# Kernel optimization log

Hardware: AMD Instinct MI355X
Metric: run time of the kernel (lower is better)

The kernel has to match this reference:

```python
import jax, jax.numpy as jnp
import numpy as np

B, T, D_IN, D_OUT, H = 4, 2048, 768, 768, 12
HD = D_OUT // H  # 64


def setup_inputs() -> dict:
    key = jax.random.key(0)
    ks = jax.random.split(key, 6)
    s_in = 1.0 / np.sqrt(D_IN)
    s_out = 1.0 / np.sqrt(D_OUT)
    return {
        "x": jax.random.normal(ks[0], (B, T, D_IN), dtype=jnp.float32),
        "Wq": jax.random.uniform(ks[1], (D_IN, D_OUT), jnp.float32, -s_in, s_in),
        "Wk": jax.random.uniform(ks[2], (D_IN, D_OUT), jnp.float32, -s_in, s_in),
        "Wv": jax.random.uniform(ks[3], (D_IN, D_OUT), jnp.float32, -s_in, s_in),
        "Wo": jax.random.uniform(ks[4], (D_OUT, D_OUT), jnp.float32, -s_out, s_out),
        "bo": jax.random.uniform(ks[5], (D_OUT,), jnp.float32, -s_out, s_out),
    }


def reference(x, Wq, Wk, Wv, Wo, bo):
    b, t, _ = x.shape
    # QKV projections (no bias, per qkv_bias=False), split into heads: [b,h,t,hd]
    q = (x @ Wq).reshape(b, t, H, HD).transpose(0, 2, 1, 3)
    k = (x @ Wk).reshape(b, t, H, HD).transpose(0, 2, 1, 3)
    v = (x @ Wv).reshape(b, t, H, HD).transpose(0, 2, 1, 3)
    # NOTE: original calls masked_fill (non-in-place) and discards the result,
    # so NO causal mask is actually applied. Faithfully reproduce that.
    scores = jnp.einsum("bhqd,bhkd->bhqk", q, k)  # [b,h,t,t]
    attn = jax.nn.softmax(scores / jnp.sqrt(jnp.float32(HD)), axis=-1)
    # dropout p=0.0 (eval) -> identity
    ctx = jnp.einsum("bhqk,bhkd->bhqd", attn, v)  # [b,h,t,hd]
    ctx = ctx.transpose(0, 2, 1, 3).reshape(b, t, D_OUT)
    return ctx @ Wo + bo
```

## Files before the change

### kernel.cpp

```cpp
#include <hip/hip_runtime.h>
#include <hip/hip_bf16.h>
#include <stdint.h>


#define HH   12
#define TT   2048
#define DIN  768
#define DOUT 768
#define HD   64
#define BB   4
#define MTOT (BB*TT)
#define NQKV (3*DOUT)
#define QSCALE 0.1803368801111832f

typedef float  float4v  __attribute__((ext_vector_type(4)));
typedef float  float16v __attribute__((ext_vector_type(16)));
typedef __bf16 bf16x8   __attribute__((ext_vector_type(8)));
typedef short  short8v  __attribute__((ext_vector_type(8)));

#define AS1 __attribute__((address_space(1)))
#define AS3 __attribute__((address_space(3)))

static __device__ __forceinline__ void gload_lds16(const void* g, void* l) {
    __builtin_amdgcn_global_load_lds((AS1 void*)g, (AS3 void*)l, 16, 0, 0);
}

static __device__ __forceinline__ short f2bf(float f) {
    __bf16 h = (__bf16)f;
    return __builtin_bit_cast(short, h);
}

__global__ __launch_bounds__(256) void prep_kernel(const float* __restrict__ x,
                                                   const float* __restrict__ Wq,
                                                   const float* __restrict__ Wk,
                                                   const float* __restrict__ Wv,
                                                   const float* __restrict__ Wo,
                                                   short* __restrict__ Xb,
                                                   short* __restrict__ Wqkvt,
                                                   short* __restrict__ Wot) {
    __shared__ short tile[32 * 33];
    const int bx = blockIdx.x, by = blockIdx.y, bz = blockIdx.z;
    if (bz == 4) {
        const int n4 = MTOT * DIN / 4;
        const int base = (by * 24 + bx) * 256 + threadIdx.x;
        for (int i = base; i < n4; i += 24 * 24 * 256) {
            float4 v = ((const float4*)x)[i];
            short4 o;
            o.x = f2bf(v.x); o.y = f2bf(v.y); o.z = f2bf(v.z); o.w = f2bf(v.w);
            ((short4*)Xb)[i] = o;
        }
        return;
    }
    const float* W = (bz == 0) ? Wq : (bz == 1) ? Wk : (bz == 2) ? Wv : Wo;
    const int tx = threadIdx.x & 31, ty = threadIdx.x >> 5;
    for (int i = 0; i < 4; i++) {
        int k = by * 32 + ty + i * 8;
        tile[(ty + i * 8) * 33 + tx] = f2bf(W[(size_t)k * DOUT + bx * 32 + tx]);
    }
    __syncthreads();
    for (int i = 0; i < 4; i++) {
        int n = bx * 32 + ty + i * 8;
        int k = by * 32 + tx;
        short v = tile[tx * 33 + ty + i * 8];
        if (bz < 3) Wqkvt[(size_t)(bz * DOUT + n) * DIN + k] = v;
        else        Wot[(size_t)n * DOUT + k] = v;
    }
}

__global__ __launch_bounds__(256) void qkv_gemm_kernel(const short* __restrict__ Xb,
                                                       const short* __restrict__ Wt,
                                                       short* __restrict__ Qb,
                                                       short* __restrict__ Kb,
                                                       short* __restrict__ Vt) {
    __shared__ __align__(16) short lds[16384];
    short* ldsA = lds;
    short* ldsB = lds + 8192;
    const int t = threadIdx.x;
    const int w = t >> 6, lane = t & 63;
    const int quad = lane >> 4, l15 = lane & 15;
    const int m0 = blockIdx.x * 128, n0 = blockIdx.y * 128;
    const int wm = (w >> 1) * 64, wn = (w & 1) * 64;

    float4v acc[4][4];
    for (int i = 0; i < 4; i++)
        for (int j = 0; j < 4; j++)
            acc[i][j] = (float4v)0.0f;

    int sOff[4];
    int sRow[4];
#pragma unroll
    for (int g = 0; g < 4; g++) {
        int slot = g * 256 + t;
        int row = slot >> 3, ch = slot & 7;
        sRow[g] = row;
        sOff[g] = ((ch ^ (row & 7)) * 8);
    }
    const int pos_r = 0;

    for (int k0 = 0; k0 < DIN; k0 += 64) {
#pragma unroll
        for (int g = 0; g < 4; g++)
            gload_lds16(Xb + (size_t)(m0 + sRow[g]) * DIN + k0 + sOff[g], &ldsA[(g * 256 + t) * 8]);
#pragma unroll
        for (int g = 0; g < 4; g++)
            gload_lds16(Wt + (size_t)(n0 + sRow[g]) * DIN + k0 + sOff[g], &ldsB[(g * 256 + t) * 8]);
        __syncthreads();
#pragma unroll
        for (int f = 0; f < 2; f++) {
            bf16x8 af[4], bfr[4];
            for (int i = 0; i < 4; i++) {
                int row = wm + i * 16 + l15;
                af[i] = *(const bf16x8*)&ldsA[row * 64 + (((f * 4 + quad) ^ (row & 7)) * 8)];
            }
            for (int j = 0; j < 4; j++) {
                int row = wn + j * 16 + l15;
                bfr[j] = *(const bf16x8*)&ldsB[row * 64 + (((f * 4 + quad) ^ (row & 7)) * 8)];
            }
            for (int i = 0; i < 4; i++)
                for (int j = 0; j < 4; j++)
                    acc[i][j] = __builtin_amdgcn_mfma_f32_16x16x32_bf16(af[i], bfr[j], acc[i][j], 0, 0, 0);
        }
        __syncthreads();
    }
    (void)pos_r;

    const int which = n0 / DOUT;
    if (which < 2) {
        short* ldsT = lds;
        const float sc = (which == 0) ? QSCALE : 1.0f;
        short* dst = (which == 0) ? Qb : Kb;
        const int n0sec = n0 - which * DOUT;
        for (int i = 0; i < 4; i++)
            for (int j = 0; j < 4; j++) {
                int col = wn + j * 16 + l15;
                int cx = col >> 3, co = col & 7;
                for (int r = 0; r < 4; r++) {
                    int row = wm + i * 16 + quad * 4 + r;
                    ldsT[row * 128 + ((cx ^ (row & 7)) * 8 + co)] = f2bf(acc[i][j][r] * sc);
                }
            }
        __syncthreads();
        for (int p = 0; p < 8; p++) {
            int row = p * 16 + (t >> 4);
            int cL = t & 15;
            short8v v = *(const short8v*)&ldsT[row * 128 + ((cL ^ (row & 7)) * 8)];
            int mg = m0 + row;
            int b2 = mg >> 11, tq = mg & 2047;
            int colg = n0sec + cL * 8;
            int hh = colg >> 6, d = colg & 63;
            *(short8v*)&dst[((size_t)((b2 * HH + hh) * TT + tq) << 6) + d] = v;
        }
    } else {
        short* ldsT = lds;
        const int n0r = n0 - 2 * DOUT;
        const int b = m0 >> 11, tq0 = m0 & 2047;
        for (int i = 0; i < 4; i++)
            for (int j = 0; j < 4; j++)
                for (int r = 0; r < 4; r++) {
                    int nl = wn + j * 16 + l15;
                    int ml = wm + i * 16 + quad * 4 + r;
                    int c = ml >> 3, o = ml & 7;
                    ldsT[nl * 128 + ((c ^ (nl & 7)) * 8 + o)] = f2bf(acc[i][j][r]);
                }
        __syncthreads();
        for (int p = 0; p < 8; p++) {
            int nrow = p * 16 + (t >> 4);
            int cc = t & 15;
            short8v v = *(const short8v*)&ldsT[nrow * 128 + ((cc ^ (nrow & 7)) * 8)];
            int colg = n0r + nrow;
            int hh = colg >> 6, d = colg & 63;
            *(short8v*)&Vt[(size_t)((b * HH + hh) * HD + d) * TT + tq0 + cc * 8] = v;
        }
    }
}

__global__ __launch_bounds__(256, 3) void attn_kernel(const short* __restrict__ Qb,
                                                      const short* __restrict__ Kb,
                                                      const short* __restrict__ Vt,
                                                      short* __restrict__ Ctx) {
    __shared__ __align__(16) short ldsK[2][64 * 64];
    __shared__ __align__(16) short ldsV[2][64 * 64];
    const int t = threadIdx.x;
    const int w = t >> 6, lane = t & 63;
    const int half = lane >> 5, m = lane & 31;
    const int bh = blockIdx.x;
    const int b = bh / HH, h = bh - b * HH;
    const int q0 = blockIdx.y * 128 + w * 32;

    const short* Qbase = Qb + (size_t)bh * TT * HD;
    const short* Kbase = Kb + (size_t)bh * TT * HD;
    const short* Vbase = Vt + (size_t)bh * HD * TT;

    bf16x8 qf[4];
#pragma unroll
    for (int s = 0; s < 4; s++)
        qf[s] = *(const bf16x8*)&Qbase[(q0 + m) * HD + s * 16 + half * 8];

    int kOff[2], vOff[2];
    {
        int r5 = t >> 3;
        int pi = ((r5 >> 3) & 1) * 16 + ((r5 >> 2) & 1) * 8 + ((r5 >> 4) & 1) * 4 + (r5 & 3);
#pragma unroll
        for (int g = 0; g < 2; g++) {
            kOff[g] = (g * 32 + pi) * 64 + (((t & 7) ^ (r5 & 7)) * 8);
            int vrow = g * 32 + r5;
            vOff[g] = vrow * TT + (((t & 7) ^ (vrow & 7)) * 8);
        }
    }

    auto stage = [&](int buf, int u0) {
#pragma unroll
        for (int g = 0; g < 2; g++)
            gload_lds16(Kbase + (size_t)u0 * 64 + kOff[g], &ldsK[buf][(g * 256 + t) * 8]);
#pragma unroll
        for (int g = 0; g < 2; g++)
            gload_lds16(Vbase + (size_t)u0 + vOff[g], &ldsV[buf][(g * 256 + t) * 8]);
    };

    float16v accO[2];
    accO[0] = (float16v)0.0f;
    accO[1] = (float16v)0.0f;
    float lsum = 0.0f;

    stage(0, 0);

    for (int it = 0; it < TT / 64; ++it) {
        __syncthreads();
        const int buf = it & 1;
        if (it + 1 < TT / 64) stage(buf ^ 1, (it + 1) * 64);
        const short* K_ = &ldsK[buf][0];
        const short* V_ = &ldsV[buf][0];

#pragma unroll
        for (int kt = 0; kt < 2; kt++) {
            float16v st = (float16v)0.0f;
#pragma unroll
            for (int s = 0; s < 4; s++) {
                bf16x8 ka = *(const bf16x8*)&K_[(kt * 32 + m) * 64 + (((s * 2 + half) ^ (m & 7)) * 8)];
                st = __builtin_amdgcn_mfma_f32_32x32x16_bf16(ka, qf[s], st, 0, 0, 0);
            }
            float pe[16];
#pragma unroll
            for (int i = 0; i < 16; i++) pe[i] = __builtin_amdgcn_exp2f(st[i]);
            float s01 = 0.0f;
#pragma unroll
            for (int i = 0; i < 16; i++) s01 += pe[i];
            lsum += s01;
            bf16x8 ap[2];
#pragma unroll
            for (int i = 0; i < 4; i++) {
                ap[0][i]     = (__bf16)pe[i];
                ap[0][4 + i] = (__bf16)pe[8 + i];
                ap[1][i]     = (__bf16)pe[4 + i];
                ap[1][4 + i] = (__bf16)pe[12 + i];
            }
#pragma unroll
            for (int ks = 0; ks < 2; ks++)
#pragma unroll
                for (int dt = 0; dt < 2; dt++) {
                    int row = dt * 32 + m;
                    bf16x8 bv = *(const bf16x8*)&V_[row * 64 + (((kt * 4 + ks * 2 + half) ^ (row & 7)) * 8)];
                    accO[dt] = __builtin_amdgcn_mfma_f32_32x32x16_bf16(ap[ks], bv, accO[dt], 0, 0, 0);
                }
        }
    }

    {
        float v = lsum + __shfl_xor(lsum, 32);
        float linv = 1.0f / v;
#pragma unroll
        for (int s = 0; s < 4; s++)
#pragma unroll
            for (int i = 0; i < 4; i++) {
                int reg = s * 4 + i;
                int qrow = i + s * 8 + half * 4;
                float ln = __shfl(linv, qrow);
                int qg = q0 + qrow;
                size_t base = (size_t)(b * TT + qg) * DOUT + h * HD + m;
                Ctx[base]      = f2bf(accO[0][reg] * ln);
                Ctx[base + 32] = f2bf(accO[1][reg] * ln);
            }
    }
}

__global__ __launch_bounds__(256) void out_gemm_kernel(const short* __restrict__ Cb,
                                                       const short* __restrict__ Wot,
                                                       const float* __restrict__ bo,
                                                       float* __restrict__ out) {
    __shared__ __align__(16) short ldsA[64 * 64];
    __shared__ __align__(16) short ldsB[128 * 64];
    const int t = threadIdx.x;
    const int w = t >> 6, lane = t & 63;
    const int quad = lane >> 4, l15 = lane & 15;
    const int m0 = blockIdx.x * 64, n0 = blockIdx.y * 128;
    const int wn = w * 32;

    float4v acc[4][2];
    for (int i = 0; i < 4; i++)
        for (int j = 0; j < 2; j++)
            acc[i][j] = (float4v)0.0f;

    for (int k0 = 0; k0 < DOUT; k0 += 64) {
#pragma unroll
        for (int g = 0; g < 2; g++) {
            int slot = g * 256 + t;
            int row = slot >> 3, ch = slot & 7;
            gload_lds16(Cb + (size_t)(m0 + row) * DOUT + k0 + ((ch ^ (row & 7)) * 8),
                        &ldsA[slot * 8]);
        }
#pragma unroll
        for (int g = 0; g < 4; g++) {
            int slot = g * 256 + t;
            int row = slot >> 3, ch = slot & 7;
            gload_lds16(Wot + (size_t)(n0 + row) * DOUT + k0 + ((ch ^ (row & 7)) * 8),
                        &ldsB[slot * 8]);
        }
        __syncthreads();
#pragma unroll
        for (int f = 0; f < 2; f++) {
            bf16x8 af[4], bfr[2];
            for (int i = 0; i < 4; i++) {
                int row = i * 16 + l15;
                af[i] = *(const bf16x8*)&ldsA[row * 64 + (((f * 4 + quad) ^ (row & 7)) * 8)];
            }
            for (int j = 0; j < 2; j++) {
                int row = wn + j * 16 + l15;
                bfr[j] = *(const bf16x8*)&ldsB[row * 64 + (((f * 4 + quad) ^ (row & 7)) * 8)];
            }
            for (int i = 0; i < 4; i++)
                for (int j = 0; j < 2; j++)
                    acc[i][j] = __builtin_amdgcn_mfma_f32_16x16x32_bf16(af[i], bfr[j], acc[i][j], 0, 0, 0);
        }
        __syncthreads();
    }

    for (int i = 0; i < 4; i++) {
        int m = m0 + i * 16 + quad * 4;
        for (int j = 0; j < 2; j++) {
            int n = n0 + wn + j * 16 + l15;
            float bias = bo[n];
            for (int r = 0; r < 4; r++)
                out[(size_t)(m + r) * DOUT + n] = acc[i][j][r] + bias;
        }
    }
}

extern "C" void kernel_launch(void* const* d_in, const int* in_sizes, int n_in,
                              void* d_out, int out_size, void* d_ws, size_t ws_size,
                              hipStream_t stream) {
    const float* x  = (const float*)d_in[0];
    const float* Wq = (const float*)d_in[1];
    const float* Wk = (const float*)d_in[2];
    const float* Wv = (const float*)d_in[3];
    const float* Wo = (const float*)d_in[4];
    const float* bo = (const float*)d_in[5];
    float* out = (float*)d_out;

    char* ws = (char*)d_ws;
    short* Xb    = (short*)(ws + 0);
    short* Wqkvt = (short*)(ws + 12582912);
    short* Wot   = (short*)(ws + 16121856);
    short* Qb    = (short*)(ws + 17301504);
    short* Kb    = (short*)(ws + 29884416);
    short* Vt    = (short*)(ws + 42467328);
    short* Cb    = (short*)(ws + 55050240);

    prep_kernel<<<dim3(24, 24, 5), 256, 0, stream>>>(x, Wq, Wk, Wv, Wo, Xb, Wqkvt, Wot);
    qkv_gemm_kernel<<<dim3(MTOT / 128, NQKV / 128), 256, 0, stream>>>(Xb, Wqkvt, Qb, Kb, Vt);
    attn_kernel<<<dim3(BB * HH, TT / 128), 256, 0, stream>>>(Qb, Kb, Vt, Cb);
    out_gemm_kernel<<<dim3(MTOT / 64, DOUT / 128), 256, 0, stream>>>(Cb, Wot, bo, out);
}
```

Baseline: 211.0 us.

## Split attention KV range across two blocks and add partial-sum reduce kernel

New measurement: 256.9 us. +21.8%, slower.

```diff
diff --git a/kernel.cpp b/kernel.cpp
--- a/kernel.cpp
+++ b/kernel.cpp
@@ -28,6 +28,9 @@
 static __device__ __forceinline__ short f2bf(float f) {
     __bf16 h = (__bf16)f;
     return __builtin_bit_cast(short, h);
+}
+static __device__ __forceinline__ float bf2f(short s) {
+    return (float)__builtin_bit_cast(__bf16, s);
 }
 
 __global__ __launch_bounds__(256) void prep_kernel(const float* __restrict__ x,
@@ -86,8 +89,7 @@
         for (int j = 0; j < 4; j++)
             acc[i][j] = (float4v)0.0f;
 
-    int sOff[4];
-    int sRow[4];
+    int sOff[4], sRow[4];
 #pragma unroll
     for (int g = 0; g < 4; g++) {
         int slot = g * 256 + t;
@@ -95,7 +97,6 @@
         sRow[g] = row;
         sOff[g] = ((ch ^ (row & 7)) * 8);
     }
-    const int pos_r = 0;
 
     for (int k0 = 0; k0 < DIN; k0 += 64) {
 #pragma unroll
@@ -122,7 +123,6 @@
         }
         __syncthreads();
     }
-    (void)pos_r;
 
     const int which = n0 / DOUT;
     if (which < 2) {
@@ -177,7 +177,9 @@
 __global__ __launch_bounds__(256, 3) void attn_kernel(const short* __restrict__ Qb,
                                                       const short* __restrict__ Kb,
                                                       const short* __restrict__ Vt,
-                                                      short* __restrict__ Ctx) {
+                                                      short* __restrict__ OP0,
+                                                      short* __restrict__ OP1,
+                                                      float* __restrict__ Lpart) {
     __shared__ __align__(16) short ldsK[2][64 * 64];
     __shared__ __align__(16) short ldsV[2][64 * 64];
     const int t = threadIdx.x;
@@ -185,16 +187,19 @@
     const int half = lane >> 5, m = lane & 31;
     const int bh = blockIdx.x;
     const int b = bh / HH, h = bh - b * HH;
-    const int q0 = blockIdx.y * 128 + w * 32;
+    const int q0 = blockIdx.y * 256 + w * 64;
+    const int kz = blockIdx.z;
 
     const short* Qbase = Qb + (size_t)bh * TT * HD;
-    const short* Kbase = Kb + (size_t)bh * TT * HD;
-    const short* Vbase = Vt + (size_t)bh * HD * TT;
-
-    bf16x8 qf[4];
-#pragma unroll
-    for (int s = 0; s < 4; s++)
-        qf[s] = *(const bf16x8*)&Qbase[(q0 + m) * HD + s * 16 + half * 8];
+    const short* Kbase = Kb + (size_t)bh * TT * HD + (size_t)kz * 1024 * HD;
+    const short* Vbase = Vt + (size_t)bh * HD * TT + (size_t)kz * 1024;
+
+    bf16x8 qf[2][4];
+#pragma unroll
+    for (int tile = 0; tile < 2; tile++)
+#pragma unroll
+        for (int s = 0; s < 4; s++)
+            qf[tile][s] = *(const bf16x8*)&Qbase[(q0 + tile * 32 + m) * HD + s * 16 + half * 8];
 
     int kOff[2], vOff[2];
     {
@@ -217,42 +222,47 @@
             gload_lds16(Vbase + (size_t)u0 + vOff[g], &ldsV[buf][(g * 256 + t) * 8]);
     };
 
-    float16v accO[2];
-    accO[0] = (float16v)0.0f;
-    accO[1] = (float16v)0.0f;
-    float lsum = 0.0f;
+    float16v accO[2][2];
+    accO[0][0] = (float16v)0.0f; accO[0][1] = (float16v)0.0f;
+    accO[1][0] = (float16v)0.0f; accO[1][1] = (float16v)0.0f;
+    float lsum[2] = {0.0f, 0.0f};
 
     stage(0, 0);
 
-    for (int it = 0; it < TT / 64; ++it) {
+    for (int it = 0; it < 16; ++it) {
         __syncthreads();
         const int buf = it & 1;
-        if (it + 1 < TT / 64) stage(buf ^ 1, (it + 1) * 64);
+        if (it + 1 < 16) stage(buf ^ 1, (it + 1) * 64);
         const short* K_ = &ldsK[buf][0];
         const short* V_ = &ldsV[buf][0];
 
 #pragma unroll
         for (int kt = 0; kt < 2; kt++) {
-            float16v st = (float16v)0.0f;
+            float16v st[2];
+            st[0] = (float16v)0.0f; st[1] = (float16v)0.0f;
 #pragma unroll
             for (int s = 0; s < 4; s++) {
                 bf16x8 ka = *(const bf16x8*)&K_[(kt * 32 + m) * 64 + (((s * 2 + half) ^ (m & 7)) * 8)];
-                st = __builtin_amdgcn_mfma_f32_32x32x16_bf16(ka, qf[s], st, 0, 0, 0);
-            }
-            float pe[16];
-#pragma unroll
-            for (int i = 0; i < 16; i++) pe[i] = __builtin_amdgcn_exp2f(st[i]);
-            float s01 = 0.0f;
-#pragma unroll
-            for (int i = 0; i < 16; i++) s01 += pe[i];
-            lsum += s01;
-            bf16x8 ap[2];
-#pragma unroll
-            for (int i = 0; i < 4; i++) {
-                ap[0][i]     = (__bf16)pe[i];
-                ap[0][4 + i] = (__bf16)pe[8 + i];
-                ap[1][i]     = (__bf16)pe[4 + i];
-                ap[1][4 + i] = (__bf16)pe[12 + i];
+                st[0] = __builtin_amdgcn_mfma_f32_32x32x16_bf16(ka, qf[0][s], st[0], 0, 0, 0);
+                st[1] = __builtin_amdgcn_mfma_f32_32x32x16_bf16(ka, qf[1][s], st[1], 0, 0, 0);
+            }
+            bf16x8 ap[2][2];
+#pragma unroll
+            for (int tile = 0; tile < 2; tile++) {
+                float pe[16];
+#pragma unroll
+                for (int i = 0; i < 16; i++) pe[i] = __builtin_amdgcn_exp2f(st[tile][i]);
+                float s01 = 0.0f;
+#pragma unroll
+                for (int i = 0; i < 16; i++) s01 += pe[i];
+                lsum[tile] += s01;
+#pragma unroll
+                for (int i = 0; i < 4; i++) {
+                    ap[tile][0][i]     = (__bf16)pe[i];
+                    ap[tile][0][4 + i] = (__bf16)pe[8 + i];
+                    ap[tile][1][i]     = (__bf16)pe[4 + i];
+                    ap[tile][1][4 + i] = (__bf16)pe[12 + i];
+                }
             }
 #pragma unroll
             for (int ks = 0; ks < 2; ks++)
@@ -260,27 +270,52 @@
                 for (int dt = 0; dt < 2; dt++) {
                     int row = dt * 32 + m;
                     bf16x8 bv = *(const bf16x8*)&V_[row * 64 + (((kt * 4 + ks * 2 + half) ^ (row & 7)) * 8)];
-                    accO[dt] = __builtin_amdgcn_mfma_f32_32x32x16_bf16(ap[ks], bv, accO[dt], 0, 0, 0);
+                    accO[0][dt] = __builtin_amdgcn_mfma_f32_32x32x16_bf16(ap[0][ks], bv, accO[0][dt], 0, 0, 0);
+                    accO[1][dt] = __builtin_amdgcn_mfma_f32_32x32x16_bf16(ap[1][ks], bv, accO[1][dt], 0, 0, 0);
                 }
         }
     }
 
-    {
-        float v = lsum + __shfl_xor(lsum, 32);
-        float linv = 1.0f / v;
+    short* OP = (kz == 0) ? OP0 : OP1;
+#pragma unroll
+    for (int tile = 0; tile < 2; tile++) {
+        float lrow = lsum[tile] + __shfl_xor(lsum[tile], 32);
+        if (half == 0)
+            Lpart[((size_t)kz * 48 + bh) * TT + q0 + tile * 32 + m] = lrow;
 #pragma unroll
         for (int s = 0; s < 4; s++)
 #pragma unroll
             for (int i = 0; i < 4; i++) {
                 int reg = s * 4 + i;
                 int qrow = i + s * 8 + half * 4;
-                float ln = __shfl(linv, qrow);
-                int qg = q0 + qrow;
+                int qg = q0 + tile * 32 + qrow;
                 size_t base = (size_t)(b * TT + qg) * DOUT + h * HD + m;
-                Ctx[base]      = f2bf(accO[0][reg] * ln);
-                Ctx[base + 32] = f2bf(accO[1][reg] * ln);
-            }
-    }
+                OP[base]      = f2bf(accO[tile][0][reg]);
+                OP[base + 32] = f2bf(accO[tile][1][reg]);
+            }
+    }
+}
+
+__global__ __launch_bounds__(256) void reduce_kernel(short* __restrict__ OP0,
+                                                     const short* __restrict__ OP1,
+                                                     const float* __restrict__ Lpart) {
+    int i8 = blockIdx.x * 256 + threadIdx.x;
+    size_t i = (size_t)i8 * 8;
+    int c = (int)(i % DOUT);
+    int qf_ = (int)(i / DOUT);
+    int b = qf_ >> 11, q = qf_ & 2047;
+    int h = c >> 6;
+    int bh = b * HH + h;
+    float l0 = Lpart[(size_t)bh * TT + q];
+    float l1 = Lpart[(size_t)(48 + bh) * TT + q];
+    float linv = 1.0f / (l0 + l1);
+    short8v a = *(const short8v*)&OP0[i];
+    short8v bb = *(const short8v*)&OP1[i];
+    short8v o;
+#pragma unroll
+    for (int j = 0; j < 8; j++)
+        o[j] = f2bf((bf2f(a[j]) + bf2f(bb[j])) * linv);
+    *(short8v*)&OP0[i] = o;
 }
 
 __global__ __launch_bounds__(256) void out_gemm_kernel(const short* __restrict__ Cb,
@@ -365,8 +400,14 @@
     short* Vt    = (short*)(ws + 42467328);
     short* Cb    = (short*)(ws + 55050240);
 
+    short* OP0   = Xb;
+    short* OP1   = Cb;
+    float* Lpart = (float*)Wqkvt;
+    short* Ctx   = OP0;
+
     prep_kernel<<<dim3(24, 24, 5), 256, 0, stream>>>(x, Wq, Wk, Wv, Wo, Xb, Wqkvt, Wot);
     qkv_gemm_kernel<<<dim3(MTOT / 128, NQKV / 128), 256, 0, stream>>>(Xb, Wqkvt, Qb, Kb, Vt);
-    attn_kernel<<<dim3(BB * HH, TT / 128), 256, 0, stream>>>(Qb, Kb, Vt, Cb);
-    out_gemm_kernel<<<dim3(MTOT / 64, DOUT / 128), 256, 0, stream>>>(Cb, Wot, bo, out);
-}
+    attn_kernel<<<dim3(BB * HH, TT / 256, 2), 256, 0, stream>>>(Qb, Kb, Vt, OP0, OP1, Lpart);
+    reduce_kernel<<<MTOT * DOUT / 8 / 256, 256, 0, stream>>>(OP0, OP1, Lpart);
+    out_gemm_kernel<<<dim3(MTOT / 64, DOUT / 128), 256, 0, stream>>>(Ctx, Wot, bo, out);
+}
```
